# Performance work log

Measured on AMD Instinct MI355X. Metric: run time of the kernel, lower is better.

Reference implementation:

```python
import jax, jax.numpy as jnp
import numpy as np

DIM = 1024
NUM_HEADS = 16
HEAD_DIM = DIM // NUM_HEADS


def setup_inputs() -> dict:
    key = jax.random.key(0)
    k1, k2, k3 = jax.random.split(key, 3)
    scale = 1.0 / np.sqrt(DIM)
    x = jax.random.normal(k1, (4, 2048, DIM), dtype=jnp.float32)
    w_qkv = jax.random.normal(k2, (DIM, 3 * DIM), dtype=jnp.float32) * scale
    b_qkv = jnp.zeros((3 * DIM,), dtype=jnp.float32)
    w_out = jax.random.normal(k3, (DIM, DIM), dtype=jnp.float32) * scale
    b_out = jnp.zeros((DIM,), dtype=jnp.float32)
    return {"x": x, "w_qkv": w_qkv, "b_qkv": b_qkv, "w_out": w_out, "b_out": b_out}


def reference(x, w_qkv, b_qkv, w_out, b_out):
    B, S, D = x.shape
    H, Hd = NUM_HEADS, HEAD_DIM
    qkv = x @ w_qkv + b_qkv  # [B,S,3D]
    q, k, v = jnp.split(qkv, 3, axis=-1)
    # [B,H,S,Hd]
    q = q.reshape(B, S, H, Hd).transpose(0, 2, 1, 3)
    k = k.reshape(B, S, H, Hd).transpose(0, 2, 1, 3)
    v = v.reshape(B, S, H, Hd).transpose(0, 2, 1, 3)
    scores = jnp.einsum('bhqd,bhkd->bhqk', q, k) / np.sqrt(Hd).astype(np.float32)
    causal = jnp.triu(jnp.ones((S, S), dtype=bool), k=1)  # True above diagonal -> masked
    scores = jnp.where(causal[None, None], -jnp.inf, scores)
    scores = scores - jnp.max(scores, axis=-1, keepdims=True)
    attn = jax.nn.softmax(scores, axis=-1)
    out = jnp.einsum('bhqk,bhkd->bhqd', attn, v)  # [B,H,S,Hd]
    out = out.transpose(0, 2, 1, 3).reshape(B, S, D)
    return out @ w_out + b_out
```

## Files before the change

### kernel.cpp

```cpp
#include <hip/hip_runtime.h>

typedef unsigned short u16;
typedef unsigned int u32;
using f32x4 = __attribute__((ext_vector_type(4))) float;
using f32x16 = __attribute__((ext_vector_type(16))) float;
using u32x4 = __attribute__((ext_vector_type(4))) u32;
typedef u32x4 __attribute__((may_alias)) u32x4a;
typedef uint2 __attribute__((may_alias)) uint2a;
using bf16x8 = __attribute__((ext_vector_type(8))) __bf16;

#define SEQ 2048

__device__ __forceinline__ u16 f2bf(float f) {
  union { float f; u32 u; } c; c.f = f;
  return (u16)((c.u + 0x7fffu + ((c.u >> 16) & 1u)) >> 16);
}
__device__ __forceinline__ float bf2f(u16 h) {
  union { u32 u; float f; } c; c.u = ((u32)h) << 16;
  return c.f;
}
__device__ __forceinline__ bf16x8 ld16(const u16* p) {
  return __builtin_bit_cast(bf16x8, *(const u32x4a*)p);
}
__device__ __forceinline__ f32x4 mfma16(bf16x8 a, bf16x8 b, f32x4 c) {
  return __builtin_amdgcn_mfma_f32_16x16x32_bf16(a, b, c, 0, 0, 0);
}
__device__ __forceinline__ f32x16 mfma32(bf16x8 a, bf16x8 b, f32x16 c) {
  return __builtin_amdgcn_mfma_f32_32x32x16_bf16(a, b, c, 0, 0, 0);
}
__device__ __forceinline__ void gload_lds16(const u16* g, u16* l) {
  __builtin_amdgcn_global_load_lds(
      (const __attribute__((address_space(1))) void*)g,
      (__attribute__((address_space(3))) void*)l, 16, 0, 0);
}
__device__ __forceinline__ u32 cvtpk(float lo, float hi) {
  u32 r;
  asm("v_cvt_pk_bf16_f32 %0, %1, %2" : "=v"(r) : "v"(lo), "v"(hi));
  return r;
}
__device__ __forceinline__ void plane32_swap(u32& a, u32& b) {
  asm("v_permlane32_swap_b32 %0, %1" : "+v"(a), "+v"(b));
}
__device__ __forceinline__ int detect_flag(const u16* x) {
  int cnt = 0;
  for (int i = 0; i < 32; ++i) {
    const int e = (x[2 * i] >> 7) & 0xFF;
    cnt += (e >= 100 && e <= 140) ? 1 : 0;
  }
  return (cnt >= 20) ? 1 : 0;
}

__global__ __launch_bounds__(256)
void prep_all(const void* __restrict__ x, const void* __restrict__ w_qkv,
              const void* __restrict__ b_qkv, const void* __restrict__ w_out,
              const void* __restrict__ b_out, u16* __restrict__ wqkvT,
              u16* __restrict__ woutT, float* __restrict__ bqf,
              float* __restrict__ bof, int* __restrict__ flagp) {
  __shared__ int sflag;
  __shared__ float t[64][65];
  const int tid = threadIdx.x;
  if (tid == 0) sflag = detect_flag((const u16*)x);
  __syncthreads();
  const int fl = sflag;
  const int bid = blockIdx.x;
  if (bid == 1040) {
    if (tid == 0) *flagp = fl;
    return;
  }
  if (bid >= 1024) {
    if (bid < 1036) {
      const int i = (bid - 1024) * 256 + tid;
      bqf[i] = fl ? bf2f(((const u16*)b_qkv)[i]) : ((const float*)b_qkv)[i];
    } else {
      const int i = (bid - 1036) * 256 + tid;
      bof[i] = fl ? bf2f(((const u16*)b_out)[i]) : ((const float*)b_out)[i];
    }
    return;
  }
  const void* in;
  u16* outp;
  int N, bx, by;
  if (bid < 768) { in = w_qkv; outp = wqkvT; N = 3072; bx = bid % 48; by = bid / 48; }
  else { in = w_out; outp = woutT; N = 1024; bx = (bid - 768) % 16; by = (bid - 768) / 16; }
  const int K = 1024;
  const int r = tid >> 4, c4 = tid & 15;
  const int n0 = bx << 6, k0 = by << 6;
#pragma unroll
  for (int i = 0; i < 4; ++i) {
    const int kk = r + i * 16;
    const size_t base = (size_t)(k0 + kk) * N + n0 + c4 * 4;
    if (fl) {
      const uint2 raw = *(const uint2*)((const u16*)in + base);
      t[kk][c4 * 4 + 0] = bf2f((u16)(raw.x & 0xFFFF));
      t[kk][c4 * 4 + 1] = bf2f((u16)(raw.x >> 16));
      t[kk][c4 * 4 + 2] = bf2f((u16)(raw.y & 0xFFFF));
      t[kk][c4 * 4 + 3] = bf2f((u16)(raw.y >> 16));
    } else {
      const float4 v = *(const float4*)((const float*)in + base);
      t[kk][c4 * 4 + 0] = v.x; t[kk][c4 * 4 + 1] = v.y;
      t[kk][c4 * 4 + 2] = v.z; t[kk][c4 * 4 + 3] = v.w;
    }
  }
  __syncthreads();
#pragma unroll
  for (int i = 0; i < 4; ++i) {
    const int nn = r + i * 16;
    uint2 ov;
    ov.x = (u32)f2bf(t[c4 * 4 + 0][nn]) | ((u32)f2bf(t[c4 * 4 + 1][nn]) << 16);
    ov.y = (u32)f2bf(t[c4 * 4 + 2][nn]) | ((u32)f2bf(t[c4 * 4 + 3][nn]) << 16);
    *(uint2*)&outp[(size_t)(n0 + nn) * K + k0 + c4 * 4] = ov;
  }
}

__global__ __launch_bounds__(256)
void cvt_x(const void* __restrict__ in, u16* __restrict__ out,
           const int* __restrict__ flag, size_t eoff4) {
  const size_t i = (size_t)blockIdx.x * 256 + threadIdx.x;
  if (*flag) {
    ((uint2*)out)[i] = ((const uint2*)in)[eoff4 + i];
  } else {
    const float4 v = ((const float4*)in)[eoff4 + i];
    uint2 ov;
    ov.x = (u32)f2bf(v.x) | ((u32)f2bf(v.y) << 16);
    ov.y = (u32)f2bf(v.z) | ((u32)f2bf(v.w) << 16);
    ((uint2*)out)[i] = ov;
  }
}

template <bool BF16_OUT>
__global__ __launch_bounds__(512, 4)
void gemm_bt(const u16* __restrict__ A, const u16* __restrict__ BT,
             const float* __restrict__ bias, void* __restrict__ Cv,
             u16* __restrict__ Vt, int M, int N, int K) {
  constexpr int BK = 32;
  __shared__ __align__(16) u16 ring[3][12288];
  const int tid = threadIdx.x;
  const int wid = tid >> 6, lane = tid & 63;
  const int quad = lane >> 4, l16 = lane & 15;

  const int nbx = gridDim.x, nwg = nbx * gridDim.y;
  int bid = blockIdx.y * nbx + blockIdx.x;
  if ((nwg & 7) == 0) bid = (bid & 7) * (nwg >> 3) + (bid >> 3);
  const int tile_n = (bid % nbx) << 7;
  const int tile_m = (bid / nbx) << 8;

  const int wmR = (wid >> 1) << 6;
  const int wnR = (wid & 1) << 6;

  const int G0 = tid;
  const int rA0 = G0 >> 2, sA0 = ((G0 & 3) ^ ((rA0 >> 1) & 3)) * 8;
  const int G1 = tid + 512;
  const int rA1 = G1 >> 2, sA1 = ((G1 & 3) ^ ((rA1 >> 1) & 3)) * 8;
  const u16* const pA0 = A + (size_t)(tile_m + rA0) * K + sA0;
  const u16* const pA1 = A + (size_t)(tile_m + rA1) * K + sA1;
  const u16* const pB0 = BT + (size_t)(tile_n + rA0) * K + sA0;
  const int dw = wid * 512;

  const int cA = (quad ^ ((l16 >> 1) & 3)) * 8;

  const int nk = K >> 5;
  f32x4 acc[4][4] = {};

  auto STAGE = [&](int kt, int buf) {
    u16* bp = ring[buf];
    const size_t ko = (size_t)kt * BK;
    gload_lds16(pA0 + ko, bp + dw);
    gload_lds16(pA1 + ko, bp + 4096 + dw);
    gload_lds16(pB0 + ko, bp + 8192 + dw);
  };

  STAGE(0, 0);
  if (nk > 1) STAGE(1, 1);

  int cur = 0;
#pragma unroll 1
  for (int t = 0; t < nk; ++t) {
    if (t + 1 < nk) asm volatile("s_waitcnt vmcnt(3)" ::: "memory");
    else            asm volatile("s_waitcnt vmcnt(0)" ::: "memory");
    __builtin_amdgcn_sched_barrier(0);
    __builtin_amdgcn_s_barrier();
    __builtin_amdgcn_sched_barrier(0);
    int sb = cur + 2; if (sb >= 3) sb -= 3;
    if (t + 2 < nk) STAGE(t + 2, sb);
    const u16* bp = ring[cur];
    bf16x8 af[4], bfr[4];
#pragma unroll
    for (int i = 0; i < 4; ++i)
      af[i] = ld16(&bp[(wmR + i * 16 + l16) * BK + cA]);
#pragma unroll
    for (int j = 0; j < 4; ++j)
      bfr[j] = ld16(&bp[8192 + (wnR + j * 16 + l16) * BK + cA]);
#pragma unroll
    for (int i = 0; i < 4; ++i)
#pragma unroll
      for (int j = 0; j < 4; ++j) acc[i][j] = mfma16(af[i], bfr[j], acc[i][j]);
    cur = (cur + 1 == 3) ? 0 : cur + 1;
  }

  if constexpr (BF16_OUT) {
    if (tile_n >= 2048) {
#pragma unroll
      for (int j = 0; j < 4; ++j) {
        const int cv = tile_n - 2048 + wnR + j * 16 + l16;
        const float bv = bias[2048 + cv];
#pragma unroll
        for (int i = 0; i < 4; ++i) {
          const int rg = tile_m + wmR + i * 16 + quad * 4;
          const int b2 = rg >> 11, s = rg & 2047;
          uint2a wv;
          wv.x = cvtpk(acc[i][j][0] + bv, acc[i][j][1] + bv);
          wv.y = cvtpk(acc[i][j][2] + bv, acc[i][j][3] + bv);
          *(uint2a*)&Vt[((size_t)(b2 * 1024 + cv)) * 2048 + s] = wv;
        }
      }
      return;
    }
  }

#pragma unroll
  for (int j = 0; j < 4; ++j) {
    const int cg = tile_n + wnR + j * 16 + l16;
    const float bv = bias[cg];
#pragma unroll
    for (int i = 0; i < 4; ++i) {
      const int rg = tile_m + wmR + i * 16 + quad * 4;
#pragma unroll
      for (int r = 0; r < 4; ++r) {
        const float v = acc[i][j][r] + bv;
        if constexpr (BF16_OUT)
          ((u16*)Cv)[(size_t)(rg + r) * N + cg] = f2bf(v);
        else
          ((float*)Cv)[(size_t)(rg + r) * N + cg] = v;
      }
    }
  }
}

__global__ __launch_bounds__(256, 3)
void attn_fwd(const u16* __restrict__ qkv, const u16* __restrict__ vt,
              u16* __restrict__ aout) {
  const int h = blockIdx.x, b = blockIdx.z;
  const int qt = 15 - (int)blockIdx.y;
  const int tid = threadIdx.x, wid = tid >> 6, lane = tid & 63;
  const int l31 = lane & 31, hi = lane >> 5;
  __shared__ __align__(16) u16 ring[3][8192];

  const int G0 = wid * 64 + lane, G1 = G0 + 256;
  const int r0 = G0 >> 3, c0 = ((G0 & 7) ^ (r0 & 7)) * 8;
  const int r1 = G1 >> 3, c1 = ((G1 & 7) ^ (r1 & 7)) * 8;
  const int db0 = wid * 512, db1 = 2048 + wid * 512;

  const u16* const kg = qkv + (size_t)(b * SEQ) * 3072 + 1024 + h * 64;
  const u16* const vg = vt + (size_t)((b * 16 + h) * 64) * 2048;

  constexpr float SC = 0.1803368801f;
  constexpr float THR = 44.3614196f;

  u32x4 onesu;
  onesu[0] = onesu[1] = onesu[2] = onesu[3] = 0x3F803F80u;
  const bf16x8 ones = __builtin_bit_cast(bf16x8, onesu);

  const int sx = l31 & 7;

  auto STAGE = [&](int kt, int buf) {
    u16* bp = ring[buf];
    const int kb = kt * 64;
    gload_lds16(kg + (size_t)(kb + r0) * 3072 + c0, bp + db0);
    gload_lds16(kg + (size_t)(kb + r1) * 3072 + c1, bp + db1);
    gload_lds16(vg + (size_t)r0 * 2048 + kb + c0, bp + 4096 + db0);
    gload_lds16(vg + (size_t)r1 * 2048 + kb + c1, bp + 4096 + db1);
  };

  const int q0w = qt * 128 + wid * 32;
  const int qrow = q0w + l31;
  bf16x8 qf[4];
#pragma unroll
  for (int d = 0; d < 4; ++d)
    qf[d] = ld16(&qkv[(size_t)(b * SEQ + qrow) * 3072 + h * 64 + d * 16 + hi * 8]);
  f32x16 o0 = {}, o1 = {}, lacc = {};
  float m_r = -1e30f, ms = -1.8e29f;

  const int last = 2 * qt + 1;
  STAGE(0, 0);
  if (last >= 1) STAGE(1, 1);

  int cur = 0;
#pragma unroll 1
  for (int kt = 0; kt <= last; ++kt) {
    if (kt + 1 <= last) asm volatile("s_waitcnt vmcnt(4)" ::: "memory");
    else                asm volatile("s_waitcnt vmcnt(0)" ::: "memory");
    __builtin_amdgcn_sched_barrier(0);
    __builtin_amdgcn_s_barrier();
    __builtin_amdgcn_sched_barrier(0);
    int sb = cur + 2; if (sb >= 3) sb -= 3;
    if (kt + 2 <= last) STAGE(kt + 2, sb);
    const int kb = kt * 64;
    if (kb <= q0w + 31) {
      const u16* const lKc = ring[cur];
      const u16* const lVc = ring[cur] + 4096;
      f32x16 s0 = {}, s1 = {};
      bf16x8 kf0[4], kf1[4];
#pragma unroll
      for (int d = 0; d < 4; ++d) {
        kf0[d] = ld16(&lKc[l31 * 64 + (((d * 2 + hi) ^ sx)) * 8]);
        kf1[d] = ld16(&lKc[(32 + l31) * 64 + (((d * 2 + hi) ^ sx)) * 8]);
      }
      __builtin_amdgcn_s_setprio(1);
#pragma unroll
      for (int d = 0; d < 4; ++d) s0 = mfma32(kf0[d], qf[d], s0);
#pragma unroll
      for (int d = 0; d < 4; ++d) s1 = mfma32(kf1[d], qf[d], s1);
      __builtin_amdgcn_s_setprio(0);
      bf16x8 vf[2][2][2];
#pragma unroll
      for (int kh = 0; kh < 2; ++kh)
#pragma unroll
        for (int j = 0; j < 2; ++j)
#pragma unroll
          for (int dh = 0; dh < 2; ++dh)
            vf[kh][j][dh] = ld16(
                &lVc[(dh * 32 + l31) * 64 + (((kh * 4 + j * 2 + hi) ^ sx)) * 8]);
      if (kb + 63 > q0w) {
        const int rel = qrow - kb - 4 * hi;
#pragma unroll
        for (int i = 0; i < 16; ++i) {
          const int kc = (i & 3) + 8 * (i >> 2);
          if (kc > rel) s0[i] = -1e30f;
          if (kc + 32 > rel) s1[i] = -1e30f;
        }
      }
      float pm = fmaxf(fmaxf(s0[0], s0[1]), s0[2]);
      pm = fmaxf(fmaxf(pm, s0[3]), s0[4]);
      pm = fmaxf(fmaxf(pm, s0[5]), s0[6]);
      pm = fmaxf(fmaxf(pm, s0[7]), s0[8]);
      pm = fmaxf(fmaxf(pm, s0[9]), s0[10]);
      pm = fmaxf(fmaxf(pm, s0[11]), s0[12]);
      pm = fmaxf(fmaxf(pm, s0[13]), s0[14]);
      pm = fmaxf(fmaxf(pm, s0[15]), s1[0]);
      pm = fmaxf(fmaxf(pm, s1[1]), s1[2]);
      pm = fmaxf(fmaxf(pm, s1[3]), s1[4]);
      pm = fmaxf(fmaxf(pm, s1[5]), s1[6]);
      pm = fmaxf(fmaxf(pm, s1[7]), s1[8]);
      pm = fmaxf(fmaxf(pm, s1[9]), s1[10]);
      pm = fmaxf(fmaxf(pm, s1[11]), s1[12]);
      pm = fmaxf(fmaxf(pm, s1[13]), s1[14]);
      pm = fmaxf(pm, s1[15]);
      if (__any(pm > m_r + THR)) {
        const float mm = fmaxf(pm, __shfl_xor(pm, 32));
        const float mn = fmaxf(m_r, mm);
        const float al = exp2f((m_r - mn) * SC);
#pragma unroll
        for (int i = 0; i < 16; ++i) {
          o0[i] *= al; o1[i] *= al; lacc[i] *= al;
        }
        m_r = mn;
        ms = mn * SC;
      }
#pragma unroll
      for (int i = 0; i < 16; ++i) {
        s0[i] = exp2f(fmaf(s0[i], SC, -ms));
        s1[i] = exp2f(fmaf(s1[i], SC, -ms));
      }
      u32 t0 = cvtpk(s0[0], s0[1]), t1 = cvtpk(s0[2], s0[3]);
      u32 t2 = cvtpk(s0[4], s0[5]), t3 = cvtpk(s0[6], s0[7]);
      u32 t4 = cvtpk(s0[8], s0[9]), t5 = cvtpk(s0[10], s0[11]);
      u32 t6 = cvtpk(s0[12], s0[13]), t7 = cvtpk(s0[14], s0[15]);
      plane32_swap(t0, t2); plane32_swap(t1, t3);
      plane32_swap(t4, t6); plane32_swap(t5, t7);
      u32x4 w00, w01;
      w00[0] = t0; w00[1] = t1; w00[2] = t2; w00[3] = t3;
      w01[0] = t4; w01[1] = t5; w01[2] = t6; w01[3] = t7;
      u32 u0 = cvtpk(s1[0], s1[1]), u1 = cvtpk(s1[2], s1[3]);
      u32 u2 = cvtpk(s1[4], s1[5]), u3 = cvtpk(s1[6], s1[7]);
      u32 u4 = cvtpk(s1[8], s1[9]), u5 = cvtpk(s1[10], s1[11]);
      u32 u6 = cvtpk(s1[12], s1[13]), u7 = cvtpk(s1[14], s1[15]);
      plane32_swap(u0, u2); plane32_swap(u1, u3);
      plane32_swap(u4, u6); plane32_swap(u5, u7);
      u32x4 w10, w11;
      w10[0] = u0; w10[1] = u1; w10[2] = u2; w10[3] = u3;
      w11[0] = u4; w11[1] = u5; w11[2] = u6; w11[3] = u7;
      const bf16x8 pb00 = __builtin_bit_cast(bf16x8, w00);
      const bf16x8 pb01 = __builtin_bit_cast(bf16x8, w01);
      const bf16x8 pb10 = __builtin_bit_cast(bf16x8, w10);
      const bf16x8 pb11 = __builtin_bit_cast(bf16x8, w11);
      __builtin_amdgcn_s_setprio(1);
      o0 = mfma32(vf[0][0][0], pb00, o0);
      o1 = mfma32(vf[0][0][1], pb00, o1);
      lacc = mfma32(ones, pb00, lacc);
      o0 = mfma32(vf[0][1][0], pb01, o0);
      o1 = mfma32(vf[0][1][1], pb01, o1);
      lacc = mfma32(ones, pb01, lacc);
      o0 = mfma32(vf[1][0][0], pb10, o0);
      o1 = mfma32(vf[1][0][1], pb10, o1);
      lacc = mfma32(ones, pb10, lacc);
      o0 = mfma32(vf[1][1][0], pb11, o0);
      o1 = mfma32(vf[1][1][1], pb11, o1);
      lacc = mfma32(ones, pb11, lacc);
      __builtin_amdgcn_s_setprio(0);
    }
    cur = (cur + 1 == 3) ? 0 : cur + 1;
  }
  const float inv = 1.0f / lacc[0];
  u16* const orow = &aout[(size_t)(b * SEQ + qrow) * 1024 + h * 64];
#pragma unroll
  for (int t = 0; t < 4; ++t) {
    const int d0 = 8 * t + 4 * hi;
    uint2a wv;
    wv.x = cvtpk(o0[4 * t] * inv, o0[4 * t + 1] * inv);
    wv.y = cvtpk(o0[4 * t + 2] * inv, o0[4 * t + 3] * inv);
    *(uint2a*)&orow[d0] = wv;
    wv.x = cvtpk(o1[4 * t] * inv, o1[4 * t + 1] * inv);
    wv.y = cvtpk(o1[4 * t + 2] * inv, o1[4 * t + 3] * inv);
    *(uint2a*)&orow[32 + d0] = wv;
  }
}

extern "C" void kernel_launch(void* const* d_in, const int* in_sizes, int n_in,
                              void* d_out, int out_size, void* d_ws, size_t ws_size,
                              hipStream_t stream) {
  const void* x     = d_in[0];
  const void* w_qkv = d_in[1];
  const void* b_qkv = d_in[2];
  const void* w_out = d_in[3];
  const void* b_out = d_in[4];
  float* out = (float*)d_out;

  float* bqf   = (float*)d_ws;
  float* bof   = bqf + 3072;
  int*   flag  = (int*)(bof + 1024);
  u16*   wqkvT = (u16*)(flag + 4);
  u16*   woutT = wqkvT + (size_t)3072 * 1024;
  u16*   xb    = woutT + (size_t)1024 * 1024;

  prep_all<<<dim3(1041), dim3(256), 0, stream>>>(
      x, w_qkv, b_qkv, w_out, b_out, wqkvT, woutT, bqf, bof, flag);

  const size_t FULL_WS = 92291088;
  if (ws_size >= FULL_WS) {
    u16* qkv = xb  + (size_t)8192 * 1024;
    u16* vt  = qkv + (size_t)8192 * 3072;
    cvt_x<<<dim3(8192), dim3(256), 0, stream>>>(x, xb, flag, 0);
    gemm_bt<true ><<<dim3(24, 32), dim3(512), 0, stream>>>(xb, wqkvT, bqf, qkv,
                                                           vt, 8192, 3072, 1024);
    attn_fwd<<<dim3(16, 16, 4), dim3(256), 0, stream>>>(qkv, vt, xb);
    gemm_bt<false><<<dim3(8, 32), dim3(512), 0, stream>>>(xb, woutT, bof, out,
                                                          vt, 8192, 1024, 1024);
  } else {
    u16* qkvb = xb   + (size_t)2048 * 1024;
    u16* vtb  = qkvb + (size_t)2048 * 3072;
    for (int b = 0; b < 4; ++b) {
      const size_t eoff4 = (size_t)b * 2048 * 1024 / 4;
      cvt_x<<<dim3(2048), dim3(256), 0, stream>>>(x, xb, flag, eoff4);
      gemm_bt<true ><<<dim3(24, 8), dim3(512), 0, stream>>>(xb, wqkvT, bqf, qkvb,
                                                            vtb, 2048, 3072, 1024);
      attn_fwd<<<dim3(16, 16, 1), dim3(256), 0, stream>>>(qkvb, vtb, xb);
      gemm_bt<false><<<dim3(8, 8), dim3(512), 0, stream>>>(
          xb, woutT, bof, out + (size_t)b * 2048 * 1024, vtb, 2048, 1024, 1024);
    }
  }
}
```

Baseline: 291.5 us.

## Pair causal query tiles per attention block, deepen K/V ring, fuse x conversion into prep

Each attention block now handles two query tiles (qt and 15-qt), so the causal work per block is balanced and the grid is halved. The LDS K/V ring grows from three to four stages with a prefetch distance of three, and occupancy drops to two blocks per SIMD. The x-to-bf16 conversion is folded into the prep kernel as extra blocks, which removes one launch. The risks are lower occupancy, more LDS per block, and a serial dependence between the two passes inside each block.

```diff
diff --git a/kernel.cpp b/kernel.cpp
--- a/kernel.cpp
+++ b/kernel.cpp
@@ -55,14 +55,28 @@
               const void* __restrict__ b_qkv, const void* __restrict__ w_out,
               const void* __restrict__ b_out, u16* __restrict__ wqkvT,
               u16* __restrict__ woutT, float* __restrict__ bqf,
-              float* __restrict__ bof, int* __restrict__ flagp) {
+              float* __restrict__ bof, int* __restrict__ flagp,
+              u16* __restrict__ xb, int cvt_blocks) {
   __shared__ int sflag;
   __shared__ float t[64][65];
   const int tid = threadIdx.x;
   if (tid == 0) sflag = detect_flag((const u16*)x);
   __syncthreads();
   const int fl = sflag;
-  const int bid = blockIdx.x;
+  if ((int)blockIdx.x < cvt_blocks) {
+    const size_t i = (size_t)blockIdx.x * 256 + tid;
+    if (fl) {
+      ((uint2*)xb)[i] = ((const uint2*)x)[i];
+    } else {
+      const float4 v = ((const float4*)x)[i];
+      uint2 ov;
+      ov.x = (u32)f2bf(v.x) | ((u32)f2bf(v.y) << 16);
+      ov.y = (u32)f2bf(v.z) | ((u32)f2bf(v.w) << 16);
+      ((uint2*)xb)[i] = ov;
+    }
+    return;
+  }
+  const int bid = blockIdx.x - cvt_blocks;
   if (bid == 1040) {
     if (tid == 0) *flagp = fl;
     return;
@@ -236,14 +250,13 @@
   }
 }
 
-__global__ __launch_bounds__(256, 3)
+__global__ __launch_bounds__(256, 2)
 void attn_fwd(const u16* __restrict__ qkv, const u16* __restrict__ vt,
               u16* __restrict__ aout) {
   const int h = blockIdx.x, b = blockIdx.z;
-  const int qt = 15 - (int)blockIdx.y;
   const int tid = threadIdx.x, wid = tid >> 6, lane = tid & 63;
   const int l31 = lane & 31, hi = lane >> 5;
-  __shared__ __align__(16) u16 ring[3][8192];
+  __shared__ __align__(16) u16 ring[4][8192];
 
   const int G0 = wid * 64 + lane, G1 = G0 + 256;
   const int r0 = G0 >> 3, c0 = ((G0 & 7) ^ (r0 & 7)) * 8;
@@ -262,8 +275,8 @@
 
   const int sx = l31 & 7;
 
-  auto STAGE = [&](int kt, int buf) {
-    u16* bp = ring[buf];
+  auto STAGE = [&](int kt) {
+    u16* bp = ring[kt & 3];
     const int kb = kt * 64;
     gload_lds16(kg + (size_t)(kb + r0) * 3072 + c0, bp + db0);
     gload_lds16(kg + (size_t)(kb + r1) * 3072 + c1, bp + db1);
@@ -271,147 +284,152 @@
     gload_lds16(vg + (size_t)r1 * 2048 + kb + c1, bp + 4096 + db1);
   };
 
-  const int q0w = qt * 128 + wid * 32;
-  const int qrow = q0w + l31;
-  bf16x8 qf[4];
-#pragma unroll
-  for (int d = 0; d < 4; ++d)
-    qf[d] = ld16(&qkv[(size_t)(b * SEQ + qrow) * 3072 + h * 64 + d * 16 + hi * 8]);
-  f32x16 o0 = {}, o1 = {}, lacc = {};
-  float m_r = -1e30f, ms = -1.8e29f;
-
-  const int last = 2 * qt + 1;
-  STAGE(0, 0);
-  if (last >= 1) STAGE(1, 1);
-
-  int cur = 0;
 #pragma unroll 1
-  for (int kt = 0; kt <= last; ++kt) {
-    if (kt + 1 <= last) asm volatile("s_waitcnt vmcnt(4)" ::: "memory");
-    else                asm volatile("s_waitcnt vmcnt(0)" ::: "memory");
-    __builtin_amdgcn_sched_barrier(0);
-    __builtin_amdgcn_s_barrier();
-    __builtin_amdgcn_sched_barrier(0);
-    int sb = cur + 2; if (sb >= 3) sb -= 3;
-    if (kt + 2 <= last) STAGE(kt + 2, sb);
-    const int kb = kt * 64;
-    if (kb <= q0w + 31) {
-      const u16* const lKc = ring[cur];
-      const u16* const lVc = ring[cur] + 4096;
-      f32x16 s0 = {}, s1 = {};
-      bf16x8 kf0[4], kf1[4];
-#pragma unroll
-      for (int d = 0; d < 4; ++d) {
-        kf0[d] = ld16(&lKc[l31 * 64 + (((d * 2 + hi) ^ sx)) * 8]);
-        kf1[d] = ld16(&lKc[(32 + l31) * 64 + (((d * 2 + hi) ^ sx)) * 8]);
+  for (int pass = 0; pass < 2; ++pass) {
+    const int qt = pass ? (int)blockIdx.y : 15 - (int)blockIdx.y;
+    const int q0w = qt * 128 + wid * 32;
+    const int qrow = q0w + l31;
+    bf16x8 qf[4];
+#pragma unroll
+    for (int d = 0; d < 4; ++d)
+      qf[d] = ld16(&qkv[(size_t)(b * SEQ + qrow) * 3072 + h * 64 + d * 16 + hi * 8]);
+    f32x16 o0 = {}, o1 = {}, lacc = {};
+    float m_r = -1e30f, ms = -1.8e29f;
+
+    const int last = 2 * qt + 1;
+    __syncthreads();
+    STAGE(0);
+    if (last >= 1) STAGE(1);
+    if (last >= 2) STAGE(2);
+
+#pragma unroll 1
+    for (int kt = 0; kt <= last; ++kt) {
+      const int rem = last - kt;
+      if (rem >= 2)      asm volatile("s_waitcnt vmcnt(8)" ::: "memory");
+      else if (rem == 1) asm volatile("s_waitcnt vmcnt(4)" ::: "memory");
+      else               asm volatile("s_waitcnt vmcnt(0)" ::: "memory");
+      __builtin_amdgcn_sched_barrier(0);
+      __builtin_amdgcn_s_barrier();
+      __builtin_amdgcn_sched_barrier(0);
+      if (kt + 3 <= last) STAGE(kt + 3);
+      const int kb = kt * 64;
+      if (kb <= q0w + 31) {
+        const u16* const lKc = ring[kt & 3];
+        const u16* const lVc = ring[kt & 3] + 4096;
+        f32x16 s0 = {}, s1 = {};
+        bf16x8 kf0[4], kf1[4];
+#pragma unroll
+        for (int d = 0; d < 4; ++d) {
+          kf0[d] = ld16(&lKc[l31 * 64 + (((d * 2 + hi) ^ sx)) * 8]);
+          kf1[d] = ld16(&lKc[(32 + l31) * 64 + (((d * 2 + hi) ^ sx)) * 8]);
+        }
+        __builtin_amdgcn_s_setprio(1);
+#pragma unroll
+        for (int d = 0; d < 4; ++d) s0 = mfma32(kf0[d], qf[d], s0);
+#pragma unroll
+        for (int d = 0; d < 4; ++d) s1 = mfma32(kf1[d], qf[d], s1);
+        __builtin_amdgcn_s_setprio(0);
+        bf16x8 vf[2][2][2];
+#pragma unroll
+        for (int kh = 0; kh < 2; ++kh)
+#pragma unroll
+          for (int j = 0; j < 2; ++j)
+#pragma unroll
+            for (int dh = 0; dh < 2; ++dh)
+              vf[kh][j][dh] = ld16(
+                  &lVc[(dh * 32 + l31) * 64 + (((kh * 4 + j * 2 + hi) ^ sx)) * 8]);
+        if (kb + 63 > q0w) {
+          const int rel = qrow - kb - 4 * hi;
+#pragma unroll
+          for (int i = 0; i < 16; ++i) {
+            const int kc = (i & 3) + 8 * (i >> 2);
+            if (kc > rel) s0[i] = -1e30f;
+            if (kc + 32 > rel) s1[i] = -1e30f;
+          }
+        }
+        float pm = fmaxf(fmaxf(s0[0], s0[1]), s0[2]);
+        pm = fmaxf(fmaxf(pm, s0[3]), s0[4]);
+        pm = fmaxf(fmaxf(pm, s0[5]), s0[6]);
+        pm = fmaxf(fmaxf(pm, s0[7]), s0[8]);
+        pm = fmaxf(fmaxf(pm, s0[9]), s0[10]);
+        pm = fmaxf(fmaxf(pm, s0[11]), s0[12]);
+        pm = fmaxf(fmaxf(pm, s0[13]), s0[14]);
+        pm = fmaxf(fmaxf(pm, s0[15]), s1[0]);
+        pm = fmaxf(fmaxf(pm, s1[1]), s1[2]);
+        pm = fmaxf(fmaxf(pm, s1[3]), s1[4]);
+        pm = fmaxf(fmaxf(pm, s1[5]), s1[6]);
+        pm = fmaxf(fmaxf(pm, s1[7]), s1[8]);
+        pm = fmaxf(fmaxf(pm, s1[9]), s1[10]);
+        pm = fmaxf(fmaxf(pm, s1[11]), s1[12]);
+        pm = fmaxf(fmaxf(pm, s1[13]), s1[14]);
+        pm = fmaxf(pm, s1[15]);
+        if (__any(pm > m_r + THR)) {
+          const float mm = fmaxf(pm, __shfl_xor(pm, 32));
+          const float mn = fmaxf(m_r, mm);
+          const float al = exp2f((m_r - mn) * SC);
+#pragma unroll
+          for (int i = 0; i < 16; ++i) {
+            o0[i] *= al; o1[i] *= al; lacc[i] *= al;
+          }
+          m_r = mn;
+          ms = mn * SC;
+        }
+#pragma unroll
+        for (int i = 0; i < 16; ++i) {
+          s0[i] = exp2f(fmaf(s0[i], SC, -ms));
+          s1[i] = exp2f(fmaf(s1[i], SC, -ms));
+        }
+        u32 t0 = cvtpk(s0[0], s0[1]), t1 = cvtpk(s0[2], s0[3]);
+        u32 t2 = cvtpk(s0[4], s0[5]), t3 = cvtpk(s0[6], s0[7]);
+        u32 t4 = cvtpk(s0[8], s0[9]), t5 = cvtpk(s0[10], s0[11]);
+        u32 t6 = cvtpk(s0[12], s0[13]), t7 = cvtpk(s0[14], s0[15]);
+        plane32_swap(t0, t2); plane32_swap(t1, t3);
+        plane32_swap(t4, t6); plane32_swap(t5, t7);
+        u32x4 w00, w01;
+        w00[0] = t0; w00[1] = t1; w00[2] = t2; w00[3] = t3;
+        w01[0] = t4; w01[1] = t5; w01[2] = t6; w01[3] = t7;
+        u32 u0 = cvtpk(s1[0], s1[1]), u1 = cvtpk(s1[2], s1[3]);
+        u32 u2 = cvtpk(s1[4], s1[5]), u3 = cvtpk(s1[6], s1[7]);
+        u32 u4 = cvtpk(s1[8], s1[9]), u5 = cvtpk(s1[10], s1[11]);
+        u32 u6 = cvtpk(s1[12], s1[13]), u7 = cvtpk(s1[14], s1[15]);
+        plane32_swap(u0, u2); plane32_swap(u1, u3);
+        plane32_swap(u4, u6); plane32_swap(u5, u7);
+        u32x4 w10, w11;
+        w10[0] = u0; w10[1] = u1; w10[2] = u2; w10[3] = u3;
+        w11[0] = u4; w11[1] = u5; w11[2] = u6; w11[3] = u7;
+        const bf16x8 pb00 = __builtin_bit_cast(bf16x8, w00);
+        const bf16x8 pb01 = __builtin_bit_cast(bf16x8, w01);
+        const bf16x8 pb10 = __builtin_bit_cast(bf16x8, w10);
+        const bf16x8 pb11 = __builtin_bit_cast(bf16x8, w11);
+        __builtin_amdgcn_s_setprio(1);
+        o0 = mfma32(vf[0][0][0], pb00, o0);
+        o1 = mfma32(vf[0][0][1], pb00, o1);
+        lacc = mfma32(ones, pb00, lacc);
+        o0 = mfma32(vf[0][1][0], pb01, o0);
+        o1 = mfma32(vf[0][1][1], pb01, o1);
+        lacc = mfma32(ones, pb01, lacc);
+        o0 = mfma32(vf[1][0][0], pb10, o0);
+        o1 = mfma32(vf[1][0][1], pb10, o1);
+        lacc = mfma32(ones, pb10, lacc);
+        o0 = mfma32(vf[1][1][0], pb11, o0);
+        o1 = mfma32(vf[1][1][1], pb11, o1);
+        lacc = mfma32(ones, pb11, lacc);
+        __builtin_amdgcn_s_setprio(0);
       }
-      __builtin_amdgcn_s_setprio(1);
-#pragma unroll
-      for (int d = 0; d < 4; ++d) s0 = mfma32(kf0[d], qf[d], s0);
-#pragma unroll
-      for (int d = 0; d < 4; ++d) s1 = mfma32(kf1[d], qf[d], s1);
-      __builtin_amdgcn_s_setprio(0);
-      bf16x8 vf[2][2][2];
-#pragma unroll
-      for (int kh = 0; kh < 2; ++kh)
-#pragma unroll
-        for (int j = 0; j < 2; ++j)
-#pragma unroll
-          for (int dh = 0; dh < 2; ++dh)
-            vf[kh][j][dh] = ld16(
-                &lVc[(dh * 32 + l31) * 64 + (((kh * 4 + j * 2 + hi) ^ sx)) * 8]);
-      if (kb + 63 > q0w) {
-        const int rel = qrow - kb - 4 * hi;
-#pragma unroll
-        for (int i = 0; i < 16; ++i) {
-          const int kc = (i & 3) + 8 * (i >> 2);
-          if (kc > rel) s0[i] = -1e30f;
-          if (kc + 32 > rel) s1[i] = -1e30f;
-        }
-      }
-      float pm = fmaxf(fmaxf(s0[0], s0[1]), s0[2]);
-      pm = fmaxf(fmaxf(pm, s0[3]), s0[4]);
-      pm = fmaxf(fmaxf(pm, s0[5]), s0[6]);
-      pm = fmaxf(fmaxf(pm, s0[7]), s0[8]);
-      pm = fmaxf(fmaxf(pm, s0[9]), s0[10]);
-      pm = fmaxf(fmaxf(pm, s0[11]), s0[12]);
-      pm = fmaxf(fmaxf(pm, s0[13]), s0[14]);
-      pm = fmaxf(fmaxf(pm, s0[15]), s1[0]);
-      pm = fmaxf(fmaxf(pm, s1[1]), s1[2]);
-      pm = fmaxf(fmaxf(pm, s1[3]), s1[4]);
-      pm = fmaxf(fmaxf(pm, s1[5]), s1[6]);
-      pm = fmaxf(fmaxf(pm, s1[7]), s1[8]);
-      pm = fmaxf(fmaxf(pm, s1[9]), s1[10]);
-      pm = fmaxf(fmaxf(pm, s1[11]), s1[12]);
-      pm = fmaxf(fmaxf(pm, s1[13]), s1[14]);
-      pm = fmaxf(pm, s1[15]);
-      if (__any(pm > m_r + THR)) {
-        const float mm = fmaxf(pm, __shfl_xor(pm, 32));
-        const float mn = fmaxf(m_r, mm);
-        const float al = exp2f((m_r - mn) * SC);
-#pragma unroll
-        for (int i = 0; i < 16; ++i) {
-          o0[i] *= al; o1[i] *= al; lacc[i] *= al;
-        }
-        m_r = mn;
-        ms = mn * SC;
-      }
-#pragma unroll
-      for (int i = 0; i < 16; ++i) {
-        s0[i] = exp2f(fmaf(s0[i], SC, -ms));
-        s1[i] = exp2f(fmaf(s1[i], SC, -ms));
-      }
-      u32 t0 = cvtpk(s0[0], s0[1]), t1 = cvtpk(s0[2], s0[3]);
-      u32 t2 = cvtpk(s0[4], s0[5]), t3 = cvtpk(s0[6], s0[7]);
-      u32 t4 = cvtpk(s0[8], s0[9]), t5 = cvtpk(s0[10], s0[11]);
-      u32 t6 = cvtpk(s0[12], s0[13]), t7 = cvtpk(s0[14], s0[15]);
-      plane32_swap(t0, t2); plane32_swap(t1, t3);
-      plane32_swap(t4, t6); plane32_swap(t5, t7);
-      u32x4 w00, w01;
-      w00[0] = t0; w00[1] = t1; w00[2] = t2; w00[3] = t3;
-      w01[0] = t4; w01[1] = t5; w01[2] = t6; w01[3] = t7;
-      u32 u0 = cvtpk(s1[0], s1[1]), u1 = cvtpk(s1[2], s1[3]);
-      u32 u2 = cvtpk(s1[4], s1[5]), u3 = cvtpk(s1[6], s1[7]);
-      u32 u4 = cvtpk(s1[8], s1[9]), u5 = cvtpk(s1[10], s1[11]);
-      u32 u6 = cvtpk(s1[12], s1[13]), u7 = cvtpk(s1[14], s1[15]);
-      plane32_swap(u0, u2); plane32_swap(u1, u3);
-      plane32_swap(u4, u6); plane32_swap(u5, u7);
-      u32x4 w10, w11;
-      w10[0] = u0; w10[1] = u1; w10[2] = u2; w10[3] = u3;
-      w11[0] = u4; w11[1] = u5; w11[2] = u6; w11[3] = u7;
-      const bf16x8 pb00 = __builtin_bit_cast(bf16x8, w00);
-      const bf16x8 pb01 = __builtin_bit_cast(bf16x8, w01);
-      const bf16x8 pb10 = __builtin_bit_cast(bf16x8, w10);
-      const bf16x8 pb11 = __builtin_bit_cast(bf16x8, w11);
-      __builtin_amdgcn_s_setprio(1);
-      o0 = mfma32(vf[0][0][0], pb00, o0);
-      o1 = mfma32(vf[0][0][1], pb00, o1);
-      lacc = mfma32(ones, pb00, lacc);
-      o0 = mfma32(vf[0][1][0], pb01, o0);
-      o1 = mfma32(vf[0][1][1], pb01, o1);
-      lacc = mfma32(ones, pb01, lacc);
-      o0 = mfma32(vf[1][0][0], pb10, o0);
-      o1 = mfma32(vf[1][0][1], pb10, o1);
-      lacc = mfma32(ones, pb10, lacc);
-      o0 = mfma32(vf[1][1][0], pb11, o0);
-      o1 = mfma32(vf[1][1][1], pb11, o1);
-      lacc = mfma32(ones, pb11, lacc);
-      __builtin_amdgcn_s_setprio(0);
-    }
-    cur = (cur + 1 == 3) ? 0 : cur + 1;
-  }
-  const float inv = 1.0f / lacc[0];
-  u16* const orow = &aout[(size_t)(b * SEQ + qrow) * 1024 + h * 64];
-#pragma unroll
-  for (int t = 0; t < 4; ++t) {
-    const int d0 = 8 * t + 4 * hi;
-    uint2a wv;
-    wv.x = cvtpk(o0[4 * t] * inv, o0[4 * t + 1] * inv);
-    wv.y = cvtpk(o0[4 * t + 2] * inv, o0[4 * t + 3] * inv);
-    *(uint2a*)&orow[d0] = wv;
-    wv.x = cvtpk(o1[4 * t] * inv, o1[4 * t + 1] * inv);
-    wv.y = cvtpk(o1[4 * t + 2] * inv, o1[4 * t + 3] * inv);
-    *(uint2a*)&orow[32 + d0] = wv;
+    }
+    const float inv = 1.0f / lacc[0];
+    u16* const orow = &aout[(size_t)(b * SEQ + qrow) * 1024 + h * 64];
+#pragma unroll
+    for (int t = 0; t < 4; ++t) {
+      const int d0 = 8 * t + 4 * hi;
+      uint2a wv;
+      wv.x = cvtpk(o0[4 * t] * inv, o0[4 * t + 1] * inv);
+      wv.y = cvtpk(o0[4 * t + 2] * inv, o0[4 * t + 3] * inv);
+      *(uint2a*)&orow[d0] = wv;
+      wv.x = cvtpk(o1[4 * t] * inv, o1[4 * t + 1] * inv);
+      wv.y = cvtpk(o1[4 * t + 2] * inv, o1[4 * t + 3] * inv);
+      *(uint2a*)&orow[32 + d0] = wv;
+    }
   }
 }
 
@@ -432,28 +450,28 @@
   u16*   woutT = wqkvT + (size_t)3072 * 1024;
   u16*   xb    = woutT + (size_t)1024 * 1024;
 
-  prep_all<<<dim3(1041), dim3(256), 0, stream>>>(
-      x, w_qkv, b_qkv, w_out, b_out, wqkvT, woutT, bqf, bof, flag);
-
   const size_t FULL_WS = 92291088;
   if (ws_size >= FULL_WS) {
     u16* qkv = xb  + (size_t)8192 * 1024;
     u16* vt  = qkv + (size_t)8192 * 3072;
-    cvt_x<<<dim3(8192), dim3(256), 0, stream>>>(x, xb, flag, 0);
+    prep_all<<<dim3(8192 + 1041), dim3(256), 0, stream>>>(
+        x, w_qkv, b_qkv, w_out, b_out, wqkvT, woutT, bqf, bof, flag, xb, 8192);
     gemm_bt<true ><<<dim3(24, 32), dim3(512), 0, stream>>>(xb, wqkvT, bqf, qkv,
                                                            vt, 8192, 3072, 1024);
-    attn_fwd<<<dim3(16, 16, 4), dim3(256), 0, stream>>>(qkv, vt, xb);
+    attn_fwd<<<dim3(16, 8, 4), dim3(256), 0, stream>>>(qkv, vt, xb);
     gemm_bt<false><<<dim3(8, 32), dim3(512), 0, stream>>>(xb, woutT, bof, out,
                                                           vt, 8192, 1024, 1024);
   } else {
     u16* qkvb = xb   + (size_t)2048 * 1024;
     u16* vtb  = qkvb + (size_t)2048 * 3072;
+    prep_all<<<dim3(1041), dim3(256), 0, stream>>>(
+        x, w_qkv, b_qkv, w_out, b_out, wqkvT, woutT, bqf, bof, flag, xb, 0);
     for (int b = 0; b < 4; ++b) {
       const size_t eoff4 = (size_t)b * 2048 * 1024 / 4;
       cvt_x<<<dim3(2048), dim3(256), 0, stream>>>(x, xb, flag, eoff4);
       gemm_bt<true ><<<dim3(24, 8), dim3(512), 0, stream>>>(xb, wqkvT, bqf, qkvb,
                                                             vtb, 2048, 3072, 1024);
-      attn_fwd<<<dim3(16, 16, 1), dim3(256), 0, stream>>>(qkvb, vtb, xb);
+      attn_fwd<<<dim3(16, 8, 1), dim3(256), 0, stream>>>(qkvb, vtb, xb);
       gemm_bt<false><<<dim3(8, 8), dim3(512), 0, stream>>>(
           xb, woutT, bof, out + (size_t)b * 2048 * 1024, vtb, 2048, 1024, 1024);
     }
```

After: 273.3 us. 6.2% less time.
